# Kernel tuning notes

Measured on AMD Instinct MI355X. Metric: run time of the kernel, lower is better.

Reference implementation:

```python
import jax, jax.numpy as jnp
import numpy as np

EPS = 1e-6

def rmsnorm(x):
    # RMSNormalize: x / sqrt(mean(x^2) + eps) over last dim (no learnable scale)
    return x * jax.lax.rsqrt(jnp.mean(jnp.square(x), axis=-1, keepdims=True) + EPS)

def setup_inputs() -> dict:
    key = jax.random.key(0)
    ks = jax.random.split(key, 7)
    B, S, D, H = 8, 4096, 1024, 128
    x = jax.random.normal(ks[0], (B, S, D), dtype=jnp.float32)
    # nn.Linear init scale ~ 1/sqrt(fan_in)
    W0 = jax.random.normal(ks[1], (D, H), dtype=jnp.float32) / np.sqrt(D)
    b0 = jax.random.normal(ks[2], (H,), dtype=jnp.float32) / np.sqrt(D)
    W1 = jax.random.normal(ks[3], (H, H), dtype=jnp.float32) / np.sqrt(H)
    b1 = jax.random.normal(ks[4], (H,), dtype=jnp.float32) / np.sqrt(H)
    W2 = jax.random.normal(ks[5], (H, H), dtype=jnp.float32) / np.sqrt(H)
    b2 = jax.random.normal(ks[6], (H,), dtype=jnp.float32) / np.sqrt(H)
    return {"x": x, "W0": W0, "b0": b0, "W1": W1, "b1": b1, "W2": W2, "b2": b2}

def reference(x, W0, b0, W1, b1, W2, b2):
    h = jnp.einsum('bsd,dh->bsh', x, W0) + b0          # linear(in_features -> 128)
    h = rmsnorm(h)                                      # RMSNormalize
    h = jax.nn.sigmoid(jnp.einsum('bsh,hk->bsk', h, W1) + b1) + h  # sigmoid block + residual
    h = jax.nn.relu(jnp.einsum('bsh,hk->bsk', h, W2) + b2) + h     # relu block + residual
    return h
```

## Files before the change

### kernel.cpp

```cpp
#include <hip/hip_runtime.h>
#include <hip/hip_bf16.h>


using u16    = unsigned short;
using f32x4  = __attribute__((ext_vector_type(4))) float;
using bf16x8 = __attribute__((ext_vector_type(8))) short;
using u16x8  = __attribute__((ext_vector_type(8))) unsigned short;

__device__ __forceinline__ float bf2f(u16 u) {
  union { unsigned int i; float f; } v; v.i = ((unsigned int)u) << 16; return v.f;
}
__device__ __forceinline__ u16 f2bf(float f) {
  union { float f; unsigned int i; } v; v.f = f;
  unsigned int r = v.i + 0x7fffu + ((v.i >> 16) & 1u);
  return (u16)(r >> 16);
}

#define WS_W0T 64
#define WS_W1T 262208
#define WS_W2T 294976
#define WS_BIAS 327744

__device__ __forceinline__ int hoff(int row, int col) {
  return row * 256 + (((col >> 3) ^ (row & 7)) << 4) + ((col & 7) << 1);
}

__global__ void __launch_bounds__(256)
prep_kernel(const float* __restrict__ W0, const float* __restrict__ W1,
            const float* __restrict__ W2, const float* __restrict__ b0,
            const float* __restrict__ b1, const float* __restrict__ b2,
            char* __restrict__ wsb) {
  const int bid = blockIdx.x;
  if (bid == 160) {
    float* bias = (float*)(wsb + WS_BIAS);
    for (int i = threadIdx.x; i < 384; i += 256) {
      int which = i >> 7, j = i & 127;
      const float* src = (which == 0) ? b0 : (which == 1) ? b1 : b2;
      bias[i] = src[j];
    }
    return;
  }
  __shared__ float tile[32][33];
  const float* src; u16* dst; int K, N, kt, nt;
  if (bid < 128)      { src = W0; dst = (u16*)(wsb + WS_W0T); K = 1024; N = 128; kt = bid >> 2;         nt = bid & 3; }
  else if (bid < 144) { src = W1; dst = (u16*)(wsb + WS_W1T); K = 128;  N = 128; kt = (bid - 128) >> 2; nt = (bid - 128) & 3; }
  else                { src = W2; dst = (u16*)(wsb + WS_W2T); K = 128;  N = 128; kt = (bid - 144) >> 2; nt = (bid - 144) & 3; }
  const int tx = threadIdx.x & 31, ty = threadIdx.x >> 5;
#pragma unroll
  for (int i = 0; i < 4; ++i) {
    int k = kt * 32 + ty + i * 8, n = nt * 32 + tx;
    tile[ty + i * 8][tx] = src[(size_t)k * N + n];
  }
  __syncthreads();
#pragma unroll
  for (int i = 0; i < 4; ++i) {
    int n = nt * 32 + ty + i * 8, k = kt * 32 + tx;
    dst[(size_t)n * K + k] = f2bf(tile[tx][ty + i * 8]);
  }
}

__global__ void __launch_bounds__(512, 4)
fused_kernel(const float* __restrict__ xin, const char* __restrict__ wsb,
             float* __restrict__ outv) {
  __shared__ char smem[49152];
  char* hns = smem;
  char* h1s = smem + 16384;

  const u16* w0t    = (const u16*)(wsb + WS_W0T);
  const u16* w1t    = (const u16*)(wsb + WS_W1T);
  const u16* w2t    = (const u16*)(wsb + WS_W2T);
  const float* bias = (const float*)(wsb + WS_BIAS);

  const int tid    = threadIdx.x;
  const int lane   = tid & 63;
  const int wave   = tid >> 6;
  const int lane16 = lane & 15;
  const int quad   = lane >> 4;
  const int m_base = (wave & 1) * 32;
  const int n_base = (wave >> 1) * 32;
  const int row0   = blockIdx.x * 64;

  const int rx  = tid >> 3;
  const int cx  = tid & 7;
  const int xsw = (cx ^ (rx & 7)) << 4;

  f32x4 xA0, xA1, xB0, xB1;
  u16x8 wA0, wA1, wB0, wB1;

  auto preload = [&](f32x4& x0, f32x4& x1, u16x8& w0, u16x8& w1, int k0) {
    const float* p = xin + (size_t)(row0 + rx) * 1024 + k0 + cx * 8;
    x0 = *(const f32x4*)p;
    x1 = *(const f32x4*)(p + 4);
    const u16* wp = w0t + (size_t)rx * 1024 + k0 + cx * 8;
    w0 = *(const u16x8*)wp;
    w1 = *(const u16x8*)(wp + 65536);
  };

  auto stage = [&](char* xs, char* wsm, const f32x4& x0, const f32x4& x1,
                   const u16x8& w0, const u16x8& w1) {
    u16x8 t;
#pragma unroll
    for (int e = 0; e < 4; ++e) { t[e] = f2bf(x0[e]); t[e + 4] = f2bf(x1[e]); }
    *(u16x8*)(xs + rx * 128 + xsw) = t;
    *(u16x8*)(wsm + rx * 128 + xsw) = w0;
    *(u16x8*)(wsm + (rx + 64) * 128 + xsw) = w1;
  };

  f32x4 acc[2][2] = {};

  auto mmac = [&](const char* xs, const char* wsm) {
#pragma unroll
    for (int kk = 0; kk < 2; ++kk) {
      int ph = ((kk * 4 + quad) ^ (lane & 7)) << 4;
      bf16x8 a[2], b[2];
#pragma unroll
      for (int rh = 0; rh < 2; ++rh)
        a[rh] = *(const bf16x8*)(xs + (m_base + rh * 16 + lane16) * 128 + ph);
#pragma unroll
      for (int nt = 0; nt < 2; ++nt)
        b[nt] = *(const bf16x8*)(wsm + (n_base + nt * 16 + lane16) * 128 + ph);
#pragma unroll
      for (int rh = 0; rh < 2; ++rh)
#pragma unroll
        for (int nt = 0; nt < 2; ++nt)
          acc[rh][nt] = __builtin_amdgcn_mfma_f32_16x16x32_bf16(
              a[rh], b[nt], acc[rh][nt], 0, 0, 0);
    }
  };

  float b0v[2];
#pragma unroll
  for (int nt = 0; nt < 2; ++nt) b0v[nt] = bias[n_base + nt * 16 + lane16];

  preload(xA0, xA1, wA0, wA1, 0);
  preload(xB0, xB1, wB0, wB1, 64);

  for (int ss = 0; ss < 8; ++ss) {
    const int s0 = ss * 2;
    stage(smem, smem + 8192, xA0, xA1, wA0, wA1);
    if (s0 + 2 < 16) preload(xA0, xA1, wA0, wA1, (s0 + 2) * 64);
    __syncthreads();
    mmac(smem, smem + 8192);

    stage(smem + 24576, smem + 32768, xB0, xB1, wB0, wB1);
    if (s0 + 3 < 16) preload(xB0, xB1, wB0, wB1, (s0 + 3) * 64);
    __syncthreads();
    mmac(smem + 24576, smem + 32768);
  }

#pragma unroll
  for (int rh = 0; rh < 2; ++rh)
#pragma unroll
    for (int nt = 0; nt < 2; ++nt) {
      int col = n_base + nt * 16 + lane16;
#pragma unroll
      for (int r = 0; r < 4; ++r) {
        int row = m_base + rh * 16 + quad * 4 + r;
        *(u16*)(hns + hoff(row, col)) = f2bf(acc[rh][nt][r] + b0v[nt]);
      }
    }
  __syncthreads();

  {
    int r = tid >> 3, q = tid & 7;
    u16x8 vals[2];
    float sum = 0.f;
#pragma unroll
    for (int j = 0; j < 2; ++j) {
      int c = q * 2 + j;
      vals[j] = *(const u16x8*)(hns + r * 256 + ((c ^ (r & 7)) << 4));
#pragma unroll
      for (int e = 0; e < 8; ++e) { float f = bf2f(vals[j][e]); sum += f * f; }
    }
    sum += __shfl_xor(sum, 1);
    sum += __shfl_xor(sum, 2);
    sum += __shfl_xor(sum, 4);
    float scale = rsqrtf(sum * (1.f / 128.f) + 1e-6f);
#pragma unroll
    for (int j = 0; j < 2; ++j) {
      u16x8 o;
#pragma unroll
      for (int e = 0; e < 8; ++e) o[e] = f2bf(bf2f(vals[j][e]) * scale);
      int c = q * 2 + j;
      *(u16x8*)(hns + r * 256 + ((c ^ (r & 7)) << 4)) = o;
    }
  }
  __syncthreads();

  float b1v[2];
#pragma unroll
  for (int nt = 0; nt < 2; ++nt) b1v[nt] = bias[128 + n_base + nt * 16 + lane16];
  f32x4 acc1[2][2] = {};
#pragma unroll
  for (int kk = 0; kk < 4; ++kk) {
    int ph = ((kk * 4 + quad) ^ (lane & 7)) << 4;
    bf16x8 a[2], b[2];
#pragma unroll
    for (int rh = 0; rh < 2; ++rh)
      a[rh] = *(const bf16x8*)(hns + (m_base + rh * 16 + lane16) * 256 + ph);
#pragma unroll
    for (int nt = 0; nt < 2; ++nt)
      b[nt] = *(const bf16x8*)(w1t + (size_t)(n_base + nt * 16 + lane16) * 128 +
                               kk * 32 + quad * 8);
#pragma unroll
    for (int rh = 0; rh < 2; ++rh)
#pragma unroll
      for (int nt = 0; nt < 2; ++nt)
        acc1[rh][nt] = __builtin_amdgcn_mfma_f32_16x16x32_bf16(
            a[rh], b[nt], acc1[rh][nt], 0, 0, 0);
  }
#pragma unroll
  for (int rh = 0; rh < 2; ++rh)
#pragma unroll
    for (int nt = 0; nt < 2; ++nt) {
      int col = n_base + nt * 16 + lane16;
#pragma unroll
      for (int r = 0; r < 4; ++r) {
        int row = m_base + rh * 16 + quad * 4 + r;
        int o = hoff(row, col);
        float hn = bf2f(*(const u16*)(hns + o));
        float v = acc1[rh][nt][r] + b1v[nt];
        *(u16*)(h1s + o) = f2bf(hn + 1.f / (1.f + __expf(-v)));
      }
    }
  __syncthreads();

  float b2v[2];
#pragma unroll
  for (int nt = 0; nt < 2; ++nt) b2v[nt] = bias[256 + n_base + nt * 16 + lane16];
  f32x4 acc2[2][2] = {};
#pragma unroll
  for (int kk = 0; kk < 4; ++kk) {
    int ph = ((kk * 4 + quad) ^ (lane & 7)) << 4;
    bf16x8 a[2], b[2];
#pragma unroll
    for (int rh = 0; rh < 2; ++rh)
      a[rh] = *(const bf16x8*)(h1s + (m_base + rh * 16 + lane16) * 256 + ph);
#pragma unroll
    for (int nt = 0; nt < 2; ++nt)
      b[nt] = *(const bf16x8*)(w2t + (size_t)(n_base + nt * 16 + lane16) * 128 +
                               kk * 32 + quad * 8);
#pragma unroll
    for (int rh = 0; rh < 2; ++rh)
#pragma unroll
      for (int nt = 0; nt < 2; ++nt)
        acc2[rh][nt] = __builtin_amdgcn_mfma_f32_16x16x32_bf16(
            a[rh], b[nt], acc2[rh][nt], 0, 0, 0);
  }
#pragma unroll
  for (int rh = 0; rh < 2; ++rh)
#pragma unroll
    for (int nt = 0; nt < 2; ++nt) {
      int col = n_base + nt * 16 + lane16;
#pragma unroll
      for (int r = 0; r < 4; ++r) {
        int row = m_base + rh * 16 + quad * 4 + r;
        float h1v = bf2f(*(const u16*)(h1s + hoff(row, col)));
        float v = acc2[rh][nt][r] + b2v[nt];
        float res = h1v + fmaxf(v, 0.f);
        outv[(size_t)(row0 + row) * 128 + col] = res;
      }
    }
}

extern "C" void kernel_launch(void* const* d_in, const int* in_sizes, int n_in,
                              void* d_out, int out_size, void* d_ws, size_t ws_size,
                              hipStream_t stream) {
  const float* x  = (const float*)d_in[0];
  const float* W0 = (const float*)d_in[1];
  const float* b0 = (const float*)d_in[2];
  const float* W1 = (const float*)d_in[3];
  const float* b1 = (const float*)d_in[4];
  const float* W2 = (const float*)d_in[5];
  const float* b2 = (const float*)d_in[6];
  char* wsb = (char*)d_ws;

  prep_kernel<<<161, 256, 0, stream>>>(W0, W1, W2, b0, b1, b2, wsb);
  fused_kernel<<<512, 512, 0, stream>>>(x, wsb, (float*)d_out);
}
```

Before: 219.4 us.

## Halve row tile per block and load W0 fragments directly into registers

The fused kernel now runs 1024 blocks of 256 threads, each covering 32 rows, instead of 512 blocks of 512 threads covering 64 rows. Each wave owns a 32-column slice across all rows of the tile. W0 fragments are no longer staged through LDS: they are prefetched from global memory straight into registers in MFMA operand layout, double-buffered alongside the x tiles. This cuts LDS use and LDS write traffic and allows more resident blocks. The cost is that each block now reads the full W0 from L2 for only half as many rows, doubling total weight reads and raising register pressure.

```diff
diff --git a/kernel.cpp b/kernel.cpp
--- a/kernel.cpp
+++ b/kernel.cpp
@@ -59,12 +59,14 @@
   }
 }
 
-__global__ void __launch_bounds__(512, 4)
+__global__ void __launch_bounds__(256, 4)
 fused_kernel(const float* __restrict__ xin, const char* __restrict__ wsb,
              float* __restrict__ outv) {
-  __shared__ char smem[49152];
-  char* hns = smem;
-  char* h1s = smem + 16384;
+  __shared__ char smem[24576];
+  char* bufA = smem;
+  char* bufB = smem + 4096;
+  char* hns  = smem + 8192;
+  char* h1s  = smem + 16384;
 
   const u16* w0t    = (const u16*)(wsb + WS_W0T);
   const u16* w1t    = (const u16*)(wsb + WS_W1T);
@@ -76,55 +78,53 @@
   const int wave   = tid >> 6;
   const int lane16 = lane & 15;
   const int quad   = lane >> 4;
-  const int m_base = (wave & 1) * 32;
-  const int n_base = (wave >> 1) * 32;
-  const int row0   = blockIdx.x * 64;
+  const int n_base = wave * 32;
+  const int row0   = blockIdx.x * 32;
 
   const int rx  = tid >> 3;
   const int cx  = tid & 7;
-  const int xsw = (cx ^ (rx & 7)) << 4;
+  const int xsw = ((cx ^ (rx & 7)) << 4);
 
   f32x4 xA0, xA1, xB0, xB1;
-  u16x8 wA0, wA1, wB0, wB1;
-
-  auto preload = [&](f32x4& x0, f32x4& x1, u16x8& w0, u16x8& w1, int k0) {
+  bf16x8 bA[2][2], bB[2][2];
+
+  auto preload_x = [&](f32x4& x0, f32x4& x1, int k0) {
     const float* p = xin + (size_t)(row0 + rx) * 1024 + k0 + cx * 8;
     x0 = *(const f32x4*)p;
     x1 = *(const f32x4*)(p + 4);
-    const u16* wp = w0t + (size_t)rx * 1024 + k0 + cx * 8;
-    w0 = *(const u16x8*)wp;
-    w1 = *(const u16x8*)(wp + 65536);
-  };
-
-  auto stage = [&](char* xs, char* wsm, const f32x4& x0, const f32x4& x1,
-                   const u16x8& w0, const u16x8& w1) {
+  };
+  auto preload_b = [&](bf16x8 (&bfr)[2][2], int k0) {
+#pragma unroll
+    for (int kk = 0; kk < 2; ++kk)
+#pragma unroll
+      for (int nt = 0; nt < 2; ++nt)
+        bfr[kk][nt] = *(const bf16x8*)(
+            w0t + (size_t)(n_base + nt * 16 + lane16) * 1024 + k0 +
+            (kk * 4 + quad) * 8);
+  };
+  auto stage_x = [&](char* xs, const f32x4& x0, const f32x4& x1) {
     u16x8 t;
 #pragma unroll
     for (int e = 0; e < 4; ++e) { t[e] = f2bf(x0[e]); t[e + 4] = f2bf(x1[e]); }
     *(u16x8*)(xs + rx * 128 + xsw) = t;
-    *(u16x8*)(wsm + rx * 128 + xsw) = w0;
-    *(u16x8*)(wsm + (rx + 64) * 128 + xsw) = w1;
   };
 
   f32x4 acc[2][2] = {};
 
-  auto mmac = [&](const char* xs, const char* wsm) {
+  auto mmac = [&](const char* xs, bf16x8 (&bfr)[2][2]) {
 #pragma unroll
     for (int kk = 0; kk < 2; ++kk) {
       int ph = ((kk * 4 + quad) ^ (lane & 7)) << 4;
-      bf16x8 a[2], b[2];
+      bf16x8 a[2];
 #pragma unroll
       for (int rh = 0; rh < 2; ++rh)
-        a[rh] = *(const bf16x8*)(xs + (m_base + rh * 16 + lane16) * 128 + ph);
-#pragma unroll
-      for (int nt = 0; nt < 2; ++nt)
-        b[nt] = *(const bf16x8*)(wsm + (n_base + nt * 16 + lane16) * 128 + ph);
+        a[rh] = *(const bf16x8*)(xs + (rh * 16 + lane16) * 128 + ph);
 #pragma unroll
       for (int rh = 0; rh < 2; ++rh)
 #pragma unroll
         for (int nt = 0; nt < 2; ++nt)
           acc[rh][nt] = __builtin_amdgcn_mfma_f32_16x16x32_bf16(
-              a[rh], b[nt], acc[rh][nt], 0, 0, 0);
+              a[rh], bfr[kk][nt], acc[rh][nt], 0, 0, 0);
     }
   };
 
@@ -132,20 +132,22 @@
 #pragma unroll
   for (int nt = 0; nt < 2; ++nt) b0v[nt] = bias[n_base + nt * 16 + lane16];
 
-  preload(xA0, xA1, wA0, wA1, 0);
-  preload(xB0, xB1, wB0, wB1, 64);
+  preload_x(xA0, xA1, 0);  preload_b(bA, 0);
+  preload_x(xB0, xB1, 64); preload_b(bB, 64);
 
   for (int ss = 0; ss < 8; ++ss) {
     const int s0 = ss * 2;
-    stage(smem, smem + 8192, xA0, xA1, wA0, wA1);
-    if (s0 + 2 < 16) preload(xA0, xA1, wA0, wA1, (s0 + 2) * 64);
+    stage_x(bufA, xA0, xA1);
+    if (s0 + 2 < 16) preload_x(xA0, xA1, (s0 + 2) * 64);
     __syncthreads();
-    mmac(smem, smem + 8192);
-
-    stage(smem + 24576, smem + 32768, xB0, xB1, wB0, wB1);
-    if (s0 + 3 < 16) preload(xB0, xB1, wB0, wB1, (s0 + 3) * 64);
+    mmac(bufA, bA);
+    if (s0 + 2 < 16) preload_b(bA, (s0 + 2) * 64);
+
+    stage_x(bufB, xB0, xB1);
+    if (s0 + 3 < 16) preload_x(xB0, xB1, (s0 + 3) * 64);
     __syncthreads();
-    mmac(smem + 24576, smem + 32768);
+    mmac(bufB, bB);
+    if (s0 + 3 < 16) preload_b(bB, (s0 + 3) * 64);
   }
 
 #pragma unroll
@@ -155,7 +157,7 @@
       int col = n_base + nt * 16 + lane16;
 #pragma unroll
       for (int r = 0; r < 4; ++r) {
-        int row = m_base + rh * 16 + quad * 4 + r;
+        int row = rh * 16 + quad * 4 + r;
         *(u16*)(hns + hoff(row, col)) = f2bf(acc[rh][nt][r] + b0v[nt]);
       }
     }
@@ -197,7 +199,7 @@
     bf16x8 a[2], b[2];
 #pragma unroll
     for (int rh = 0; rh < 2; ++rh)
-      a[rh] = *(const bf16x8*)(hns + (m_base + rh * 16 + lane16) * 256 + ph);
+      a[rh] = *(const bf16x8*)(hns + (rh * 16 + lane16) * 256 + ph);
 #pragma unroll
     for (int nt = 0; nt < 2; ++nt)
       b[nt] = *(const bf16x8*)(w1t + (size_t)(n_base + nt * 16 + lane16) * 128 +
@@ -216,7 +218,7 @@
       int col = n_base + nt * 16 + lane16;
 #pragma unroll
       for (int r = 0; r < 4; ++r) {
-        int row = m_base + rh * 16 + quad * 4 + r;
+        int row = rh * 16 + quad * 4 + r;
         int o = hoff(row, col);
         float hn = bf2f(*(const u16*)(hns + o));
         float v = acc1[rh][nt][r] + b1v[nt];
@@ -235,7 +237,7 @@
     bf16x8 a[2], b[2];
 #pragma unroll
     for (int rh = 0; rh < 2; ++rh)
-      a[rh] = *(const bf16x8*)(h1s + (m_base + rh * 16 + lane16) * 256 + ph);
+      a[rh] = *(const bf16x8*)(h1s + (rh * 16 + lane16) * 256 + ph);
 #pragma unroll
     for (int nt = 0; nt < 2; ++nt)
       b[nt] = *(const bf16x8*)(w2t + (size_t)(n_base + nt * 16 + lane16) * 128 +
@@ -254,7 +256,7 @@
       int col = n_base + nt * 16 + lane16;
 #pragma unroll
       for (int r = 0; r < 4; ++r) {
-        int row = m_base + rh * 16 + quad * 4 + r;
+        int row = rh * 16 + quad * 4 + r;
         float h1v = bf2f(*(const u16*)(h1s + hoff(row, col)));
         float v = acc2[rh][nt][r] + b2v[nt];
         float res = h1v + fmaxf(v, 0.f);
@@ -276,5 +278,5 @@
   char* wsb = (char*)d_ws;
 
   prep_kernel<<<161, 256, 0, stream>>>(W0, W1, W2, b0, b1, b2, wsb);
-  fused_kernel<<<512, 512, 0, stream>>>(x, wsb, (float*)d_out);
-}
+  fused_kernel<<<1024, 256, 0, stream>>>(x, wsb, (float*)d_out);
+}
```

After: 226.6 us. 1.03x slower.
